# Optimization experiments

Measured on AMD Instinct MI355X. Metric: run time of the kernel, lower is better.

The kernel has to match this reference:

```python
import jax, jax.numpy as jnp
import numpy as np

N = 4096          # n_nodes
M = 8192          # m_nodes (= 2*N, required by block structure)
D = 128           # in_dim == hidden_dim (conv1 is reapplied to its own output)
H = 128
NUM_ITERS = 3


def setup_inputs() -> dict:
    key = jax.random.key(0)
    ks = jax.random.split(key, 6)
    X = jax.random.normal(ks[0], (N, D), dtype=jnp.float32)
    R = jax.random.uniform(ks[1], (N, N), dtype=jnp.float32)
    A = 0.5 * (R + R.T)  # symmetric, strictly positive connectivity matrix
    # upsample MLP: Linear(n_nodes -> m_nodes - n_nodes), torch weight layout [out, in]
    W_up = jax.random.normal(ks[2], (M - N, N), dtype=jnp.float32) * 0.02
    b_up = jnp.zeros((M - N,), dtype=jnp.float32)
    # GCNConv linear weights stored [in, out]
    W1 = jax.random.normal(ks[3], (D, H), dtype=jnp.float32) * 0.05
    b1 = jnp.zeros((H,), dtype=jnp.float32)
    W2 = jax.random.normal(ks[4], (H, H), dtype=jnp.float32) * 0.05
    b2 = jnp.zeros((H,), dtype=jnp.float32)
    return dict(X=X, A=A, W_up=W_up, b_up=b_up, W1=W1, b1=b1, W2=W2, b2=b2)


def _gcn(Adj, X, W, b):
    # PyG GCNConv on a fully dense, strictly-positive weighted graph:
    # every diagonal entry is nonzero, so add_remaining_self_loops is a no-op and
    # out = D^{-1/2} A D^{-1/2} (X W) + b  exactly.
    deg = Adj.sum(axis=0)                         # [m] column degree
    dinv = jnp.where(deg > 0, jax.lax.rsqrt(deg), 0.0)
    An = Adj * dinv[:, None] * dinv[None, :]      # symmetric normalization
    return An @ (X @ W) + b


def reference(X, A, W_up, b_up, W1, b1, W2, b2):
    # new_nodes = upsample_mlp(X.T).T  -> [M-N, D]
    new_nodes = (X.T @ W_up.T + b_up).T
    Xu = jnp.concatenate([X, new_nodes], axis=0)  # [M, D]
    # block adjacency: [[A, A.T], [A, sigmoid(new @ new.T)]]
    Adj = jnp.block([[A, A.T],
                     [A, jax.nn.sigmoid(new_nodes @ new_nodes.T)]])  # [M, M]
    A_out = Adj
    for _ in range(NUM_ITERS):
        Xu = jax.nn.relu(_gcn(Adj, Xu, W1, b1))
        Adj = jax.nn.sigmoid(Xu @ Xu.T)           # mid-loop adjacency rebuild
        Xu = jax.nn.relu(_gcn(Adj, Xu, W2, b2))
        A_out = jax.nn.sigmoid(Xu @ Xu.T)
        # NOTE: edge_index for the next conv1 is NOT rebuilt from A_out in the
        # original (only after conv1), so Adj carries the mid-loop matrix.
    return A_out
```

## Files before the change

### kernel.cpp

```cpp
#include <hip/hip_runtime.h>
#include <hip/hip_bf16.h>


#define N_NODES 4096
#define M_NODES 8192
#define DIM 128
#define SLICE_ELEMS ((size_t)M_NODES * DIM)

typedef __attribute__((ext_vector_type(4))) float f32x4;
typedef __attribute__((ext_vector_type(8))) short bf16x8;

__device__ __forceinline__ unsigned short f2bf(float f) {
  union { float f; unsigned u; } v; v.f = f;
  unsigned r = v.u + 0x7fffu + ((v.u >> 16) & 1u);
  return (unsigned short)(r >> 16);
}

__device__ __forceinline__ void gld16(unsigned short* lds, const unsigned short* g) {
  __builtin_amdgcn_global_load_lds(
      (const __attribute__((address_space(1))) unsigned int*)g,
      (__attribute__((address_space(3))) unsigned int*)lds, 16, 0, 0);
}

__device__ __forceinline__ float sigmoidf_(float x) { return 1.0f / (1.0f + __expf(-x)); }


__global__ void cast_x_kernel(const float* __restrict__ X, unsigned short* __restrict__ Xu,
                              unsigned short* __restrict__ XT) {
  int idx = blockIdx.x * 256 + threadIdx.x;
  int i = idx >> 7, c = idx & 127;
  unsigned short b = f2bf(X[idx]);
  Xu[idx] = b;
  XT[(size_t)c * N_NODES + i] = b;
}

__global__ void cast_wup_kernel(const float4* __restrict__ W, unsigned short* __restrict__ Wb) {
  int idx4 = blockIdx.x * 256 + threadIdx.x;
  int r = idx4 >> 10, c = (idx4 & 1023) << 2;
  float4 v = W[idx4];
  ushort4 o;
  o.x = f2bf(v.x); o.y = f2bf(v.y); o.z = f2bf(v.z); o.w = f2bf(v.w);
  int tm = r >> 7, rr = r & 127;
  int kc = c >> 10, st = (c & 1023) >> 5, e = c & 31;
  *(ushort4*)&Wb[((size_t)tm * 4 + kc) * 131072 + (size_t)st * 4096 + rr * 32 + e] = o;
}

__global__ void cast_wt_kernel(const float* __restrict__ W, unsigned short* __restrict__ WT) {
  int idx = blockIdx.x * 256 + threadIdx.x;
  int k = idx >> 7, c = idx & 127;
  WT[c * DIM + k] = f2bf(W[idx]);
}

__global__ void cast_a_kernel(const float* __restrict__ A, unsigned short* __restrict__ Adj,
                              float* __restrict__ colsumA) {
  int c = blockIdx.x * 256 + threadIdx.x;
  int r0 = blockIdx.y * 128;
  int tm = r0 >> 7;
  int kc = c >> 10, st = (c & 1023) >> 5, e = c & 31;
  size_t a1 = ((size_t)(tm)      * 8 + kc)     * 131072 + (size_t)st * 4096 + e;
  size_t a2 = ((size_t)(tm)      * 8 + 4 + kc) * 131072 + (size_t)st * 4096 + e;
  size_t a3 = ((size_t)(tm + 32) * 8 + kc)     * 131072 + (size_t)st * 4096 + e;
  float s = 0.f;
  for (int r = 0; r < 128; ++r) {
    float a = A[(size_t)(r0 + r) * N_NODES + c];
    unsigned short b = f2bf(a);
    Adj[a1 + r * 32] = b; Adj[a2 + r * 32] = b; Adj[a3 + r * 32] = b;
    s += a;
  }
  atomicAdd(&colsumA[c], s);
}

__global__ void init_deg_kernel(const float* __restrict__ colsumA, float* __restrict__ deg) {
  int i = blockIdx.x * 256 + threadIdx.x;
  deg[i] = (i < N_NODES) ? 2.0f * colsumA[i] : colsumA[i - N_NODES];
}

__global__ void dinv_kernel(const float* __restrict__ deg, float* __restrict__ dinv) {
  int i = blockIdx.x * 256 + threadIdx.x;
  float d = deg[i];
  dinv[i] = d > 0.f ? rsqrtf(d) : 0.f;
}


__global__ __launch_bounds__(256, 2)
void agg_kernel(const unsigned short* __restrict__ At, long tileRowElems,
                const unsigned short* __restrict__ BT, long ldb,
                float* __restrict__ accBase, int kIters) {
  __shared__ __align__(16) unsigned short lA[4096];
  __shared__ __align__(16) unsigned short lB[4096];
  const int t = threadIdx.x, w = t >> 6, lane = t & 63;
  const int q = lane >> 4, l15 = lane & 15;
  const int sg0 = blockIdx.y * kIters;
  const size_t abase = (size_t)blockIdx.x * tileRowElems +
                       (size_t)(sg0 >> 5) * 131072 + (size_t)(sg0 & 31) * 4096;
  const size_t bk = (size_t)sg0 * 32;
  const int arow = t >> 2, achk = t & 3;

  f32x4 acc[2][8];
#pragma unroll
  for (int a = 0; a < 2; ++a)
#pragma unroll
    for (int b = 0; b < 8; ++b) acc[a][b] = (f32x4)0.f;

  for (int s = 0; s < kIters; ++s) {
    __syncthreads();
    gld16(&lA[t * 8],        &At[abase + (size_t)s * 4096 + t * 8]);
    gld16(&lA[2048 + t * 8], &At[abase + (size_t)s * 4096 + 2048 + t * 8]);
    gld16(&lB[t * 8],        &BT[(size_t)arow * ldb + bk + s * 32 + achk * 8]);
    gld16(&lB[2048 + t * 8], &BT[(size_t)(64 + arow) * ldb + bk + s * 32 + achk * 8]);
    __syncthreads();
    bf16x8 a0 = *(const bf16x8*)&lA[(w * 32 + l15) * 32 + q * 8];
    bf16x8 a1 = *(const bf16x8*)&lA[(w * 32 + 16 + l15) * 32 + q * 8];
#pragma unroll
    for (int nt = 0; nt < 8; ++nt) {
      bf16x8 b = *(const bf16x8*)&lB[(nt * 16 + l15) * 32 + q * 8];
      acc[0][nt] = __builtin_amdgcn_mfma_f32_16x16x32_bf16(a0, b, acc[0][nt], 0, 0, 0);
      acc[1][nt] = __builtin_amdgcn_mfma_f32_16x16x32_bf16(a1, b, acc[1][nt], 0, 0, 0);
    }
  }
  float* ct = accBase + (size_t)blockIdx.y * SLICE_ELEMS + (size_t)blockIdx.x * 16384;
#pragma unroll
  for (int mt = 0; mt < 2; ++mt)
#pragma unroll
    for (int nt = 0; nt < 8; ++nt)
      *(f32x4*)&ct[(((w * 2 + mt) * 8 + nt) * 256) + (q * 16 + l15) * 4] = acc[mt][nt];
}

__global__ void reduce_acc_kernel(const float* __restrict__ acc,
                                  unsigned short* __restrict__ dst,
                                  const float* __restrict__ bias_row,
                                  const float* __restrict__ bias_col,
                                  const float* __restrict__ dinv, int mode, int nSlices) {
  int p = blockIdx.x * 256 + threadIdx.x;
  float s = 0.f;
  for (int sp = 0; sp < nSlices; ++sp) s += acc[(size_t)sp * SLICE_ELEMS + p];
  int tile = p >> 14, r = p & 16383;
  int grp = r >> 8, r2 = r & 255;
  int nt = grp & 7, wmt = grp >> 3;
  int i = r2 & 3, ql = r2 >> 2;
  int row = tile * 128 + (wmt >> 1) * 32 + (wmt & 1) * 16 + (ql >> 4) * 4 + i;
  int col = nt * 16 + (ql & 15);
  float v = (mode == 0) ? (s + bias_row[row])
                        : fmaxf(dinv[row] * s + bias_col[col], 0.f);
  dst[(size_t)row * DIM + col] = f2bf(v);
}


template <int MODE>
__global__ __launch_bounds__(256)
void rebuild_kernel(const unsigned short* __restrict__ XA,
                    const unsigned short* __restrict__ XB,
                    void* __restrict__ out, long p1 ,
                    long col0, float* __restrict__ deg) {
  __shared__ __align__(16) unsigned short smem[32768];
  __shared__ float lcol[128];
  unsigned short* lA = smem;
  unsigned short* lB = smem + 16384;
  const int t = threadIdx.x, w = t >> 6, lane = t & 63;
  const int q = lane >> 4, l15 = lane & 15;
  const int i0 = blockIdx.x * 128, j0 = blockIdx.y * 128;
  const int srow = t >> 2, schk = t & 3;
#pragma unroll
  for (int kk = 0; kk < 4; ++kk)
#pragma unroll
    for (int h = 0; h < 2; ++h) {
      gld16(&lA[kk * 4096 + h * 2048 + t * 8],
            &XA[(size_t)(i0 + h * 64 + srow) * DIM + kk * 32 + schk * 8]);
      gld16(&lB[kk * 4096 + h * 2048 + t * 8],
            &XB[(size_t)(j0 + h * 64 + srow) * DIM + kk * 32 + schk * 8]);
    }
  if (MODE == 0 && t < 128) lcol[t] = 0.f;
  __syncthreads();

  f32x4 acc[2][8];
#pragma unroll
  for (int a = 0; a < 2; ++a)
#pragma unroll
    for (int b = 0; b < 8; ++b) acc[a][b] = (f32x4)0.f;

#pragma unroll
  for (int kk = 0; kk < 4; ++kk) {
    bf16x8 a0 = *(const bf16x8*)&lA[kk * 4096 + (w * 32 + l15) * 32 + q * 8];
    bf16x8 a1 = *(const bf16x8*)&lA[kk * 4096 + (w * 32 + 16 + l15) * 32 + q * 8];
#pragma unroll
    for (int nt = 0; nt < 8; ++nt) {
      bf16x8 b = *(const bf16x8*)&lB[kk * 4096 + (nt * 16 + l15) * 32 + q * 8];
      acc[0][nt] = __builtin_amdgcn_mfma_f32_16x16x32_bf16(a0, b, acc[0][nt], 0, 0, 0);
      acc[1][nt] = __builtin_amdgcn_mfma_f32_16x16x32_bf16(a1, b, acc[1][nt], 0, 0, 0);
    }
  }
  __syncthreads();

  if (MODE == 0) {
    unsigned short* lC = smem;
#pragma unroll
    for (int mt = 0; mt < 2; ++mt)
#pragma unroll
      for (int nt = 0; nt < 8; ++nt) {
        float cs = 0.f;
#pragma unroll
        for (int i = 0; i < 4; ++i) {
          float sv = sigmoidf_(acc[mt][nt][i]);
          cs += sv;
          lC[(w * 32 + mt * 16 + q * 4 + i) * 136 + nt * 16 + l15] = f2bf(sv);
        }
        cs += __shfl_xor(cs, 16);
        cs += __shfl_xor(cs, 32);
        if (lane < 16) atomicAdd(&lcol[nt * 16 + lane], cs);
      }
    __syncthreads();
    unsigned short* og = (unsigned short*)out;
    const long rowbase = p1 + i0, colbase = col0 + j0;
    const size_t tb = ((size_t)(rowbase >> 7) * 8 + (colbase >> 10)) * 131072;
    const int stb = (int)((colbase & 1023) >> 5);
#pragma unroll
    for (int cc = 0; cc < 8; ++cc) {
      int ch = t + cc * 256;
      int row = ch >> 4, c16 = ch & 15;
      *(bf16x8*)&og[tb + (size_t)(stb + (c16 >> 2)) * 4096 + row * 32 + (c16 & 3) * 8] =
          *(const bf16x8*)&lC[row * 136 + c16 * 8];
    }
    if (t < 128) atomicAdd(&deg[colbase + t], lcol[t]);
  } else {
    float* og = (float*)out;
    float* lCf = (float*)smem;
#pragma unroll
    for (int h2 = 0; h2 < 2; ++h2) {
      __syncthreads();
      if ((w >> 1) == h2) {
#pragma unroll
        for (int mt = 0; mt < 2; ++mt)
#pragma unroll
          for (int nt = 0; nt < 8; ++nt)
#pragma unroll
            for (int i = 0; i < 4; ++i)
              lCf[((w & 1) * 32 + mt * 16 + q * 4 + i) * 128 + nt * 16 + l15] =
                  sigmoidf_(acc[mt][nt][i]);
      }
      __syncthreads();
#pragma unroll
      for (int j = 0; j < 8; ++j) {
        int ch = t + j * 256;
        int r64 = ch >> 5, c4 = (ch & 31) * 4;
        *(f32x4*)&og[(size_t)(i0 + h2 * 64 + r64) * p1 + j0 + c4] =
            *(const f32x4*)&lCf[r64 * 128 + c4];
      }
    }
  }
}


__global__ __launch_bounds__(256)
void yz_kernel(const unsigned short* __restrict__ Xu, const unsigned short* __restrict__ WT,
               const float* __restrict__ dinv, unsigned short* __restrict__ ZT, int ldz) {
  __shared__ __align__(16) unsigned short smem[32768];
  unsigned short* lA = smem;
  unsigned short* lB = smem + 16384;
  const int t = threadIdx.x, w = t >> 6, lane = t & 63;
  const int q = lane >> 4, l15 = lane & 15;
  const int r0 = blockIdx.x * 128;
  const int srow = t >> 2, schk = t & 3;
#pragma unroll
  for (int kk = 0; kk < 4; ++kk)
#pragma unroll
    for (int h = 0; h < 2; ++h) {
      gld16(&lA[kk * 4096 + h * 2048 + t * 8],
            &Xu[(size_t)(r0 + h * 64 + srow) * DIM + kk * 32 + schk * 8]);
      gld16(&lB[kk * 4096 + h * 2048 + t * 8],
            &WT[(size_t)(h * 64 + srow) * DIM + kk * 32 + schk * 8]);
    }
  __syncthreads();

  f32x4 acc[2][8];
#pragma unroll
  for (int a = 0; a < 2; ++a)
#pragma unroll
    for (int b = 0; b < 8; ++b) acc[a][b] = (f32x4)0.f;

#pragma unroll
  for (int kk = 0; kk < 4; ++kk) {
    bf16x8 a0 = *(const bf16x8*)&lA[kk * 4096 + (w * 32 + l15) * 32 + q * 8];
    bf16x8 a1 = *(const bf16x8*)&lA[kk * 4096 + (w * 32 + 16 + l15) * 32 + q * 8];
#pragma unroll
    for (int nt = 0; nt < 8; ++nt) {
      bf16x8 b = *(const bf16x8*)&lB[kk * 4096 + (nt * 16 + l15) * 32 + q * 8];
      acc[0][nt] = __builtin_amdgcn_mfma_f32_16x16x32_bf16(a0, b, acc[0][nt], 0, 0, 0);
      acc[1][nt] = __builtin_amdgcn_mfma_f32_16x16x32_bf16(a1, b, acc[1][nt], 0, 0, 0);
    }
  }
  __syncthreads();
  unsigned short* lT = smem;
#pragma unroll
  for (int mt = 0; mt < 2; ++mt)
#pragma unroll
    for (int nt = 0; nt < 8; ++nt)
#pragma unroll
      for (int i = 0; i < 4; ++i) {
        int r = w * 32 + mt * 16 + q * 4 + i;
        lT[(nt * 16 + l15) * 136 + r] = f2bf(dinv[r0 + r] * acc[mt][nt][i]);
      }
  __syncthreads();
#pragma unroll
  for (int cc = 0; cc < 8; ++cc) {
    int ch = t + cc * 256;
    int c = ch >> 4, c16 = ch & 15;
    *(bf16x8*)&ZT[(size_t)c * ldz + r0 + c16 * 8] = *(const bf16x8*)&lT[c * 136 + c16 * 8];
  }
}


extern "C" void kernel_launch(void* const* d_in, const int* in_sizes, int n_in,
                              void* d_out, int out_size, void* d_ws, size_t ws_size,
                              hipStream_t stream) {
  (void)in_sizes; (void)n_in; (void)out_size;
  const float* X   = (const float*)d_in[0];
  const float* A   = (const float*)d_in[1];
  const float* Wup = (const float*)d_in[2];
  const float* bup = (const float*)d_in[3];
  const float* W1  = (const float*)d_in[4];
  const float* b1  = (const float*)d_in[5];
  const float* W2  = (const float*)d_in[6];
  const float* b2  = (const float*)d_in[7];

  const size_t ADJ_BYTES = (size_t)M_NODES * M_NODES * 2;
  char* ws = (char*)d_ws;
  size_t off = 0;
  auto alloc = [&](size_t bytes) {
    char* p = ws + off;
    off += (bytes + 255) & ~(size_t)255;
    return p;
  };
  float*          accb    = (float*)alloc(8 * SLICE_ELEMS * 4);
  unsigned short* Xu      = (unsigned short*)alloc((size_t)M_NODES * DIM * 2);
  unsigned short* ZT      = (unsigned short*)alloc((size_t)DIM * M_NODES * 2);
  unsigned short* XT      = (unsigned short*)alloc((size_t)DIM * N_NODES * 2);
  unsigned short* W1T     = (unsigned short*)alloc(DIM * DIM * 2);
  unsigned short* W2T     = (unsigned short*)alloc(DIM * DIM * 2);
  float*          colsumA = (float*)alloc(N_NODES * 4);
  float*          deg     = (float*)alloc(M_NODES * 4);
  float*          dinv    = (float*)alloc(M_NODES * 4);

  unsigned short* Adj;
  if (ws_size >= off + ADJ_BYTES) Adj = (unsigned short*)(ws + off);
  else                            Adj = (unsigned short*)d_out;
  unsigned short* Wupb = Adj;

  unsigned short* XuNew = Xu + (size_t)N_NODES * DIM;

  hipMemsetAsync(colsumA, 0, N_NODES * 4, stream);
  cast_x_kernel<<<N_NODES * DIM / 256, 256, 0, stream>>>(X, Xu, XT);
  cast_wup_kernel<<<((size_t)N_NODES * N_NODES / 4) / 256, 256, 0, stream>>>(
      (const float4*)Wup, Wupb);
  cast_wt_kernel<<<64, 256, 0, stream>>>(W1, W1T);
  cast_wt_kernel<<<64, 256, 0, stream>>>(W2, W2T);

  agg_kernel<<<dim3(N_NODES / 128, 8), 256, 0, stream>>>(
      Wupb, 4L * 131072, XT, N_NODES, accb, 16);
  reduce_acc_kernel<<<N_NODES * DIM / 256, 256, 0, stream>>>(
      accb, XuNew, bup, nullptr, nullptr, 0, 8);

  cast_a_kernel<<<dim3(N_NODES / 256, N_NODES / 128), 256, 0, stream>>>(A, Adj, colsumA);
  init_deg_kernel<<<M_NODES / 256, 256, 0, stream>>>(colsumA, deg);
  rebuild_kernel<0><<<dim3(N_NODES / 128, N_NODES / 128), 256, 0, stream>>>(
      XuNew, XuNew, Adj, N_NODES, N_NODES, deg);
  dinv_kernel<<<M_NODES / 256, 256, 0, stream>>>(deg, dinv);

  for (int it = 0; it < 3; ++it) {
    yz_kernel<<<M_NODES / 128, 256, 0, stream>>>(Xu, W1T, dinv, ZT, M_NODES);
    agg_kernel<<<dim3(M_NODES / 128, 8), 256, 0, stream>>>(
        Adj, 8L * 131072, ZT, M_NODES, accb, 32);
    reduce_acc_kernel<<<M_NODES * DIM / 256, 256, 0, stream>>>(
        accb, Xu, nullptr, b1, dinv, 1, 8);
    hipMemsetAsync(deg, 0, M_NODES * 4, stream);
    rebuild_kernel<0><<<dim3(M_NODES / 128, M_NODES / 128), 256, 0, stream>>>(
        Xu, Xu, Adj, 0, 0, deg);
    dinv_kernel<<<M_NODES / 256, 256, 0, stream>>>(deg, dinv);
    yz_kernel<<<M_NODES / 128, 256, 0, stream>>>(Xu, W2T, dinv, ZT, M_NODES);
    agg_kernel<<<dim3(M_NODES / 128, 8), 256, 0, stream>>>(
        Adj, 8L * 131072, ZT, M_NODES, accb, 32);
    reduce_acc_kernel<<<M_NODES * DIM / 256, 256, 0, stream>>>(
        accb, Xu, nullptr, b2, dinv, 1, 8);
    if (it == 2)
      rebuild_kernel<1><<<dim3(M_NODES / 128, M_NODES / 128), 256, 0, stream>>>(
          Xu, Xu, d_out, M_NODES, 0, nullptr);
  }
}
```

Baseline: 989.2 us.

## Retile adjacency into 128x128 blocks and stream agg operands directly to registers

Changes the bf16 adjacency and W_up layouts from 128x32 k-slabs to contiguous 128x128 row-major tiles. The aggregation kernel drops LDS staging and barriers, loading A and B fragments straight from global memory into registers with a two-stage software pipeline. The separate dinv kernel is removed and rsqrt of the degree is computed inline in the consumers. This cuts LDS traffic, synchronisation and launches, at the risk of less coalesced, strided global loads and more register pressure.

```diff
diff --git a/kernel.cpp b/kernel.cpp
--- a/kernel.cpp
+++ b/kernel.cpp
@@ -40,9 +40,7 @@
   float4 v = W[idx4];
   ushort4 o;
   o.x = f2bf(v.x); o.y = f2bf(v.y); o.z = f2bf(v.z); o.w = f2bf(v.w);
-  int tm = r >> 7, rr = r & 127;
-  int kc = c >> 10, st = (c & 1023) >> 5, e = c & 31;
-  *(ushort4*)&Wb[((size_t)tm * 4 + kc) * 131072 + (size_t)st * 4096 + rr * 32 + e] = o;
+  *(ushort4*)&Wb[((size_t)(r >> 7) * 32 + (c >> 7)) * 16384 + (r & 127) * 128 + (c & 127)] = o;
 }
 
 __global__ void cast_wt_kernel(const float* __restrict__ W, unsigned short* __restrict__ WT) {
@@ -55,16 +53,15 @@
                               float* __restrict__ colsumA) {
   int c = blockIdx.x * 256 + threadIdx.x;
   int r0 = blockIdx.y * 128;
-  int tm = r0 >> 7;
-  int kc = c >> 10, st = (c & 1023) >> 5, e = c & 31;
-  size_t a1 = ((size_t)(tm)      * 8 + kc)     * 131072 + (size_t)st * 4096 + e;
-  size_t a2 = ((size_t)(tm)      * 8 + 4 + kc) * 131072 + (size_t)st * 4096 + e;
-  size_t a3 = ((size_t)(tm + 32) * 8 + kc)     * 131072 + (size_t)st * 4096 + e;
+  int tm = r0 >> 7, tc = c >> 7, cl = c & 127;
+  size_t a1 = ((size_t)tm        * 64 + tc)      * 16384 + cl;
+  size_t a2 = ((size_t)tm        * 64 + 32 + tc) * 16384 + cl;
+  size_t a3 = ((size_t)(tm + 32) * 64 + tc)      * 16384 + cl;
   float s = 0.f;
   for (int r = 0; r < 128; ++r) {
     float a = A[(size_t)(r0 + r) * N_NODES + c];
     unsigned short b = f2bf(a);
-    Adj[a1 + r * 32] = b; Adj[a2 + r * 32] = b; Adj[a3 + r * 32] = b;
+    Adj[a1 + r * 128] = b; Adj[a2 + r * 128] = b; Adj[a3 + r * 128] = b;
     s += a;
   }
   atomicAdd(&colsumA[c], s);
@@ -75,26 +72,14 @@
   deg[i] = (i < N_NODES) ? 2.0f * colsumA[i] : colsumA[i - N_NODES];
 }
 
-__global__ void dinv_kernel(const float* __restrict__ deg, float* __restrict__ dinv) {
-  int i = blockIdx.x * 256 + threadIdx.x;
-  float d = deg[i];
-  dinv[i] = d > 0.f ? rsqrtf(d) : 0.f;
-}
-
 
 __global__ __launch_bounds__(256, 2)
-void agg_kernel(const unsigned short* __restrict__ At, long tileRowElems,
+void agg_kernel(const unsigned short* __restrict__ At, int tnTotal,
                 const unsigned short* __restrict__ BT, long ldb,
                 float* __restrict__ accBase, int kIters) {
-  __shared__ __align__(16) unsigned short lA[4096];
-  __shared__ __align__(16) unsigned short lB[4096];
   const int t = threadIdx.x, w = t >> 6, lane = t & 63;
   const int q = lane >> 4, l15 = lane & 15;
-  const int sg0 = blockIdx.y * kIters;
-  const size_t abase = (size_t)blockIdx.x * tileRowElems +
-                       (size_t)(sg0 >> 5) * 131072 + (size_t)(sg0 & 31) * 4096;
-  const size_t bk = (size_t)sg0 * 32;
-  const int arow = t >> 2, achk = t & 3;
+  const int tn0 = blockIdx.y * (kIters >> 2);
 
   f32x4 acc[2][8];
 #pragma unroll
@@ -102,22 +87,48 @@
 #pragma unroll
     for (int b = 0; b < 8; ++b) acc[a][b] = (f32x4)0.f;
 
-  for (int s = 0; s < kIters; ++s) {
-    __syncthreads();
-    gld16(&lA[t * 8],        &At[abase + (size_t)s * 4096 + t * 8]);
-    gld16(&lA[2048 + t * 8], &At[abase + (size_t)s * 4096 + 2048 + t * 8]);
-    gld16(&lB[t * 8],        &BT[(size_t)arow * ldb + bk + s * 32 + achk * 8]);
-    gld16(&lB[2048 + t * 8], &BT[(size_t)(64 + arow) * ldb + bk + s * 32 + achk * 8]);
-    __syncthreads();
-    bf16x8 a0 = *(const bf16x8*)&lA[(w * 32 + l15) * 32 + q * 8];
-    bf16x8 a1 = *(const bf16x8*)&lA[(w * 32 + 16 + l15) * 32 + q * 8];
-#pragma unroll
-    for (int nt = 0; nt < 8; ++nt) {
-      bf16x8 b = *(const bf16x8*)&lB[(nt * 16 + l15) * 32 + q * 8];
-      acc[0][nt] = __builtin_amdgcn_mfma_f32_16x16x32_bf16(a0, b, acc[0][nt], 0, 0, 0);
-      acc[1][nt] = __builtin_amdgcn_mfma_f32_16x16x32_bf16(a1, b, acc[1][nt], 0, 0, 0);
-    }
-  }
+  const size_t abase = ((size_t)blockIdx.x * tnTotal + tn0) * 16384 +
+                       (size_t)(w * 32 + l15) * 128 + q * 8;
+  const size_t bbase = (size_t)blockIdx.y * kIters * 32 + q * 8;
+
+  bf16x8 a0_0, a1_0, b_0[8];
+  bf16x8 a0_1, a1_1, b_1[8];
+
+#define LOADG(KT, S)                                                                \
+  do {                                                                              \
+    const int kt_ = (KT);                                                           \
+    const size_t ao_ = (size_t)(kt_ >> 2) * 16384 + (kt_ & 3) * 32;                 \
+    a0_##S = *(const bf16x8*)&At[abase + ao_];                                      \
+    a1_##S = *(const bf16x8*)&At[abase + 16 * 128 + ao_];                           \
+    _Pragma("unroll")                                                               \
+    for (int nt = 0; nt < 8; ++nt)                                                  \
+      b_##S[nt] = *(const bf16x8*)&BT[(size_t)(nt * 16 + l15) * ldb + bbase + (size_t)kt_ * 32]; \
+  } while (0)
+
+#define COMPUTE(S)                                                                  \
+  do {                                                                              \
+    _Pragma("unroll")                                                               \
+    for (int nt = 0; nt < 8; ++nt) {                                                \
+      acc[0][nt] = __builtin_amdgcn_mfma_f32_16x16x32_bf16(a0_##S, b_##S[nt], acc[0][nt], 0, 0, 0); \
+      acc[1][nt] = __builtin_amdgcn_mfma_f32_16x16x32_bf16(a1_##S, b_##S[nt], acc[1][nt], 0, 0, 0); \
+    }                                                                               \
+  } while (0)
+
+  LOADG(0, 0);
+  int kt = 0;
+#pragma unroll 1
+  for (; kt + 2 < kIters; kt += 2) {
+    LOADG(kt + 1, 1);
+    COMPUTE(0);
+    LOADG(kt + 2, 0);
+    COMPUTE(1);
+  }
+  LOADG(kt + 1, 1);
+  COMPUTE(0);
+  COMPUTE(1);
+#undef LOADG
+#undef COMPUTE
+
   float* ct = accBase + (size_t)blockIdx.y * SLICE_ELEMS + (size_t)blockIdx.x * 16384;
 #pragma unroll
   for (int mt = 0; mt < 2; ++mt)
@@ -130,7 +141,7 @@
                                   unsigned short* __restrict__ dst,
                                   const float* __restrict__ bias_row,
                                   const float* __restrict__ bias_col,
-                                  const float* __restrict__ dinv, int mode, int nSlices) {
+                                  const float* __restrict__ deg, int mode, int nSlices) {
   int p = blockIdx.x * 256 + threadIdx.x;
   float s = 0.f;
   for (int sp = 0; sp < nSlices; ++sp) s += acc[(size_t)sp * SLICE_ELEMS + p];
@@ -140,8 +151,13 @@
   int i = r2 & 3, ql = r2 >> 2;
   int row = tile * 128 + (wmt >> 1) * 32 + (wmt & 1) * 16 + (ql >> 4) * 4 + i;
   int col = nt * 16 + (ql & 15);
-  float v = (mode == 0) ? (s + bias_row[row])
-                        : fmaxf(dinv[row] * s + bias_col[col], 0.f);
+  float v;
+  if (mode == 0) v = s + bias_row[row];
+  else {
+    float d = deg[row];
+    float dv = d > 0.f ? rsqrtf(d) : 0.f;
+    v = fmaxf(dv * s + bias_col[col], 0.f);
+  }
   dst[(size_t)row * DIM + col] = f2bf(v);
 }
 
@@ -211,14 +227,12 @@
     __syncthreads();
     unsigned short* og = (unsigned short*)out;
     const long rowbase = p1 + i0, colbase = col0 + j0;
-    const size_t tb = ((size_t)(rowbase >> 7) * 8 + (colbase >> 10)) * 131072;
-    const int stb = (int)((colbase & 1023) >> 5);
+    unsigned short* tg = og + (((size_t)(rowbase >> 7)) * 64 + (colbase >> 7)) * 16384;
 #pragma unroll
     for (int cc = 0; cc < 8; ++cc) {
       int ch = t + cc * 256;
       int row = ch >> 4, c16 = ch & 15;
-      *(bf16x8*)&og[tb + (size_t)(stb + (c16 >> 2)) * 4096 + row * 32 + (c16 & 3) * 8] =
-          *(const bf16x8*)&lC[row * 136 + c16 * 8];
+      *(bf16x8*)&tg[row * 128 + c16 * 8] = *(const bf16x8*)&lC[row * 136 + c16 * 8];
     }
     if (t < 128) atomicAdd(&deg[colbase + t], lcol[t]);
   } else {
@@ -252,7 +266,7 @@
 
 __global__ __launch_bounds__(256)
 void yz_kernel(const unsigned short* __restrict__ Xu, const unsigned short* __restrict__ WT,
-               const float* __restrict__ dinv, unsigned short* __restrict__ ZT, int ldz) {
+               const float* __restrict__ deg, unsigned short* __restrict__ ZT, int ldz) {
   __shared__ __align__(16) unsigned short smem[32768];
   unsigned short* lA = smem;
   unsigned short* lB = smem + 16384;
@@ -288,6 +302,14 @@
       acc[1][nt] = __builtin_amdgcn_mfma_f32_16x16x32_bf16(a1, b, acc[1][nt], 0, 0, 0);
     }
   }
+  float dv[2][4];
+#pragma unroll
+  for (int mt = 0; mt < 2; ++mt)
+#pragma unroll
+    for (int i = 0; i < 4; ++i) {
+      float d = deg[r0 + w * 32 + mt * 16 + q * 4 + i];
+      dv[mt][i] = d > 0.f ? rsqrtf(d) : 0.f;
+    }
   __syncthreads();
   unsigned short* lT = smem;
 #pragma unroll
@@ -297,7 +319,7 @@
 #pragma unroll
       for (int i = 0; i < 4; ++i) {
         int r = w * 32 + mt * 16 + q * 4 + i;
-        lT[(nt * 16 + l15) * 136 + r] = f2bf(dinv[r0 + r] * acc[mt][nt][i]);
+        lT[(nt * 16 + l15) * 136 + r] = f2bf(dv[mt][i] * acc[mt][nt][i]);
       }
   __syncthreads();
 #pragma unroll
@@ -338,7 +360,6 @@
   unsigned short* W2T     = (unsigned short*)alloc(DIM * DIM * 2);
   float*          colsumA = (float*)alloc(N_NODES * 4);
   float*          deg     = (float*)alloc(M_NODES * 4);
-  float*          dinv    = (float*)alloc(M_NODES * 4);
 
   unsigned short* Adj;
   if (ws_size >= off + ADJ_BYTES) Adj = (unsigned short*)(ws + off);
@@ -355,7 +376,7 @@
   cast_wt_kernel<<<64, 256, 0, stream>>>(W2, W2T);
 
   agg_kernel<<<dim3(N_NODES / 128, 8), 256, 0, stream>>>(
-      Wupb, 4L * 131072, XT, N_NODES, accb, 16);
+      Wupb, 32, XT, N_NODES, accb, 16);
   reduce_acc_kernel<<<N_NODES * DIM / 256, 256, 0, stream>>>(
       accb, XuNew, bup, nullptr, nullptr, 0, 8);
 
@@ -363,23 +384,21 @@
   init_deg_kernel<<<M_NODES / 256, 256, 0, stream>>>(colsumA, deg);
   rebuild_kernel<0><<<dim3(N_NODES / 128, N_NODES / 128), 256, 0, stream>>>(
       XuNew, XuNew, Adj, N_NODES, N_NODES, deg);
-  dinv_kernel<<<M_NODES / 256, 256, 0, stream>>>(deg, dinv);
 
   for (int it = 0; it < 3; ++it) {
-    yz_kernel<<<M_NODES / 128, 256, 0, stream>>>(Xu, W1T, dinv, ZT, M_NODES);
+    yz_kernel<<<M_NODES / 128, 256, 0, stream>>>(Xu, W1T, deg, ZT, M_NODES);
     agg_kernel<<<dim3(M_NODES / 128, 8), 256, 0, stream>>>(
-        Adj, 8L * 131072, ZT, M_NODES, accb, 32);
+        Adj, 64, ZT, M_NODES, accb, 32);
     reduce_acc_kernel<<<M_NODES * DIM / 256, 256, 0, stream>>>(
-        accb, Xu, nullptr, b1, dinv, 1, 8);
+        accb, Xu, nullptr, b1, deg, 1, 8);
     hipMemsetAsync(deg, 0, M_NODES * 4, stream);
     rebuild_kernel<0><<<dim3(M_NODES / 128, M_NODES / 128), 256, 0, stream>>>(
         Xu, Xu, Adj, 0, 0, deg);
-    dinv_kernel<<<M_NODES / 256, 256, 0, stream>>>(deg, dinv);
-    yz_kernel<<<M_NODES / 128, 256, 0, stream>>>(Xu, W2T, dinv, ZT, M_NODES);
+    yz_kernel<<<M_NODES / 128, 256, 0, stream>>>(Xu, W2T, deg, ZT, M_NODES);
     agg_kernel<<<dim3(M_NODES / 128, 8), 256, 0, stream>>>(
-        Adj, 8L * 131072, ZT, M_NODES, accb, 32);
+        Adj, 64, ZT, M_NODES, accb, 32);
     reduce_acc_kernel<<<M_NODES * DIM / 256, 256, 0, stream>>>(
-        accb, Xu, nullptr, b2, dinv, 1, 8);
+        accb, Xu, nullptr, b2, deg, 1, 8);
     if (it == 2)
       rebuild_kernel<1><<<dim3(M_NODES / 128, M_NODES / 128), 256, 0, stream>>>(
           Xu, Xu, d_out, M_NODES, 0, nullptr);
```

Result: slower. 1.260 ms (+27.4%).
